# Kernel tuning notes

Measured on AMD Instinct MI355X. Metric: run time of the kernel, lower is better.

## Reference

```python
import jax, jax.numpy as jnp
import numpy as np

BPTT, BSZ, NTOKEN = 32, 32, 2000
NINP, NHID = 1024, 256


def setup_inputs() -> dict:
    key = jax.random.key(0)
    ks = jax.random.split(key, 8)
    s = 0.1  # matches uniform(-0.1, 0.1) init scale
    return {
        "input": jax.random.normal(ks[0], (BPTT, BSZ, NTOKEN), jnp.float32),
        "b": jax.random.normal(ks[1], (BSZ, NHID), jnp.float32),
        "RBF_w": jax.random.uniform(ks[2], (NINP, NTOKEN), jnp.float32, -s, s),
        "RBF_b": jnp.zeros((NINP,), jnp.float32),
        "emb_w": jax.random.uniform(ks[3], (NHID, NINP), jnp.float32, -s, s),
        "emb_b": jnp.zeros((NHID,), jnp.float32),
        "wfef_w": jax.random.uniform(ks[4], (NHID * NHID, NHID), jnp.float32, -s, s),
        "wfef_b": jnp.zeros((NHID * NHID,), jnp.float32),
        "dec_w": jax.random.uniform(ks[5], (NTOKEN, NHID), jnp.float32, -s, s),
        "dec_b": jnp.zeros((NTOKEN,), jnp.float32),
    }


def reference(input, b, RBF_w, RBF_b, emb_w, emb_b, wfef_w, wfef_b, dec_w, dec_b):
    bptt, bsz, ntoken = input.shape
    nhid = b.shape[1]
    ninp = RBF_w.shape[0]
    rbf_scale = np.float32(np.sqrt(2.0) / np.sqrt(ninp))
    # random Fourier features: cos(RBF(x)) * sqrt(2/ninp)
    encoded = jnp.cos(input @ RBF_w.T + RBF_b) * rbf_scale      # [bptt,bsz,ninp]
    obs = encoded @ emb_w.T + emb_b                              # [bptt,bsz,nhid]

    def step(b_t, obs_t):
        # per-sample transition matrix from current state
        W = (b_t @ wfef_w.T + wfef_b).reshape(bsz, nhid, nhid)   # [bsz,nhid,nhid]
        bn = jnp.einsum('brc,bc->br', W, obs_t)                  # [bsz,nhid]
        bn = bn / jnp.sqrt(jnp.sum(bn * bn, axis=1, keepdims=True))
        out = bn @ dec_w.T + dec_b                               # [bsz,ntoken]
        return bn, out

    b_final, outputs = jax.lax.scan(step, b, obs)                # outputs: [bptt,bsz,ntoken]
    return outputs, b_final
```

## Files before the change

kernel.cpp:

```cpp
#include <hip/hip_runtime.h>
#include <hip/hip_fp16.h>
#include <math.h>

typedef _Float16 half_t;
typedef __attribute__((ext_vector_type(2))) _Float16 f16x2;
typedef __attribute__((ext_vector_type(4))) _Float16 f16x4;
typedef __attribute__((ext_vector_type(8))) _Float16 f16x8;
typedef __attribute__((ext_vector_type(4))) float f32x4;

#define BPTT 32
#define BSZ 32
#define NTOK 2000
#define NTOKP 2048
#define NINP 1024
#define NHID 256
#define TB 1024
#define NH2 65536
#define TCH 8
#define FUSED_LDS 25600
#define FRONT_LDS 24576

__device__ __forceinline__ int swz(int row, int hoff) {
  return (row * 32 + hoff) ^ ((row & 7) << 3);
}

__global__ void cvtAll_k(const float* __restrict__ input, half_t* __restrict__ A1hi,
                         half_t* __restrict__ A1lo, const float* __restrict__ RBF_w,
                         half_t* __restrict__ B1hi, half_t* __restrict__ B1lo,
                         const float* __restrict__ emb_w,
                         const float* __restrict__ wfef_b,
                         const float* __restrict__ dec_w, half_t* __restrict__ B2,
                         half_t* __restrict__ WBh, half_t* __restrict__ B4) {
  int bid = blockIdx.x;
  if (bid < 16384) {
    const float* src;
    half_t *hi, *lo;
    int idx;
    if (bid < 8192) {
      src = input; hi = A1hi; lo = A1lo; idx = bid * 256 + threadIdx.x;
    } else {
      src = RBF_w; hi = B1hi; lo = B1lo; idx = (bid - 8192) * 256 + threadIdx.x;
    }
    int r = idx >> 11, c = idx & 2047;
    float v = (c < NTOK) ? src[(size_t)r * NTOK + c] : 0.f;
    half_t h = (half_t)v;
    hi[idx] = h;
    lo[idx] = (half_t)(v - (float)h);
    return;
  }
  int i = (bid - 16384) * 256 + threadIdx.x;
  if (i < 262144) { B2[i] = (half_t)emb_w[i]; return; }
  i -= 262144;
  if (i < 65536) { WBh[i] = (half_t)wfef_b[i]; return; }
  i -= 65536;
  int r = i >> 8, c = i & 255;
  B4[i] = (half_t)((r < NTOK) ? dec_w[(size_t)r * 256 + c] : 0.f);
}

template <int EP>
__global__ __launch_bounds__(256) void gemm128_k(const half_t* __restrict__ A,
                                                 const half_t* __restrict__ B,
                                                 void* __restrict__ C,
                                                 const float* __restrict__ bias, int K,
                                                 int ldc) {
  __shared__ half_t As[128 * 32];
  __shared__ half_t Bs[128 * 32];
  const int tid = threadIdx.x;
  const int lane = tid & 63, wave = tid >> 6;
  const int wr = wave >> 1, wc = wave & 1;
  const int row0 = blockIdx.x * 128, col0 = blockIdx.y * 128;
  const int srow = tid >> 2, sseg = tid & 3;
  const size_t aoff = (size_t)(row0 + srow) * K + sseg * 8;
  const size_t boff = (size_t)(col0 + srow) * K + sseg * 8;
  const int fr = lane & 15, fq = lane >> 4;

  f32x4 acc[4][4];
#pragma unroll
  for (int m = 0; m < 4; m++)
#pragma unroll
    for (int n = 0; n < 4; n++) acc[m][n] = (f32x4)(0.0f);

  for (int k0 = 0; k0 < K; k0 += 32) {
    f16x8 a0 = *(const f16x8*)(A + aoff + k0);
    f16x8 a1 = *(const f16x8*)(A + aoff + (size_t)64 * K + k0);
    f16x8 b0 = *(const f16x8*)(B + boff + k0);
    f16x8 b1 = *(const f16x8*)(B + boff + (size_t)64 * K + k0);
    __syncthreads();
    *(f16x8*)(As + swz(srow, sseg * 8)) = a0;
    *(f16x8*)(As + swz(srow + 64, sseg * 8)) = a1;
    *(f16x8*)(Bs + swz(srow, sseg * 8)) = b0;
    *(f16x8*)(Bs + swz(srow + 64, sseg * 8)) = b1;
    __syncthreads();
    f16x8 af[4], bf[4];
#pragma unroll
    for (int m = 0; m < 4; m++)
      af[m] = *(const f16x8*)(As + swz(wr * 64 + m * 16 + fr, fq * 8));
#pragma unroll
    for (int n = 0; n < 4; n++)
      bf[n] = *(const f16x8*)(Bs + swz(wc * 64 + n * 16 + fr, fq * 8));
#pragma unroll
    for (int m = 0; m < 4; m++)
#pragma unroll
      for (int n = 0; n < 4; n++)
        acc[m][n] = __builtin_amdgcn_mfma_f32_16x16x32_f16(af[m], bf[n], acc[m][n], 0, 0, 0);
  }

#pragma unroll
  for (int m = 0; m < 4; m++)
#pragma unroll
    for (int n = 0; n < 4; n++)
#pragma unroll
      for (int j = 0; j < 4; j++) {
        int gr = row0 + wr * 64 + m * 16 + fq * 4 + j;
        int gc = col0 + wc * 64 + n * 16 + fr;
        float v = acc[m][n][j];
        if (EP == 1) {
          ((half_t*)C)[(size_t)gr * ldc + gc] = (half_t)(v + bias[gc]);
        } else {
          ((float*)C)[(size_t)gr * ldc + gc] = v;
        }
      }
}

template <int EP>
__device__ __forceinline__ void gemmMC_body(const half_t* __restrict__ A,
                                            const half_t* __restrict__ B,
                                            void* __restrict__ C,
                                            const float* __restrict__ bias, int col0,
                                            int ldc, int nvalid, char* smem) {
  half_t* As = (half_t*)smem;
  half_t* Bs = (half_t*)(smem + 16384);
  const int tid = threadIdx.x;
  const int lane = tid & 63, wave = tid >> 6;
  const int wr = wave >> 2, wc = wave & 3;
  const int srow = tid >> 2, sseg = tid & 3;
  const int fr = lane & 15, fq = lane >> 4;
  const size_t aoff = (size_t)srow * 256 + sseg * 8;
  const size_t boff = (size_t)(col0 + (srow & 127)) * 256 + sseg * 8;

  f32x4 acc[4][2];
#pragma unroll
  for (int m = 0; m < 4; m++)
#pragma unroll
    for (int n = 0; n < 2; n++) acc[m][n] = (f32x4)(0.0f);

  for (int k0 = 0; k0 < 256; k0 += 32) {
    f16x8 a0 = *(const f16x8*)(A + aoff + k0);
    f16x8 b0;
    if (tid < 512) b0 = *(const f16x8*)(B + boff + k0);
    __syncthreads();
    *(f16x8*)(As + swz(srow, sseg * 8)) = a0;
    if (tid < 512) *(f16x8*)(Bs + swz(srow, sseg * 8)) = b0;
    __syncthreads();
    f16x8 af[4], bf[2];
#pragma unroll
    for (int m = 0; m < 4; m++)
      af[m] = *(const f16x8*)(As + swz(wr * 64 + m * 16 + fr, fq * 8));
#pragma unroll
    for (int n = 0; n < 2; n++)
      bf[n] = *(const f16x8*)(Bs + swz(wc * 32 + n * 16 + fr, fq * 8));
#pragma unroll
    for (int m = 0; m < 4; m++)
#pragma unroll
      for (int n = 0; n < 2; n++)
        acc[m][n] = __builtin_amdgcn_mfma_f32_16x16x32_f16(af[m], bf[n], acc[m][n], 0, 0, 0);
  }

#pragma unroll
  for (int m = 0; m < 4; m++)
#pragma unroll
    for (int n = 0; n < 2; n++)
#pragma unroll
      for (int j = 0; j < 4; j++) {
        int gr = wr * 64 + m * 16 + fq * 4 + j;
        int gc = col0 + wc * 32 + n * 16 + fr;
        if (EP == 0) {
          ((half_t*)C)[(size_t)gr * ldc + gc] = (half_t)acc[m][n][j];
        } else {
          if (gc < nvalid)
            ((float*)C)[(size_t)gr * ldc + gc] = acc[m][n][j] + bias[gc];
        }
      }
}

__device__ void scan_body(const half_t* __restrict__ Mc, const float* __restrict__ V,
                          int t0, const float* __restrict__ bin,
                          float* __restrict__ bstate, half_t* __restrict__ BN,
                          float* __restrict__ bfinal, int b, char* smem) {
  float(*Vs)[256] = (float(*)[256])smem;
  float(*partial)[260] = (float(*)[260])(smem + 8192);
  unsigned* bh2 = (unsigned*)(smem + 24832);
  float* red = (float*)(smem + 25344);
  const int tid = threadIdx.x;
  const int hh = tid >> 6, lane = tid & 63;
  const int hpar = lane >> 5, r8 = (lane & 31) * 8;

  if (tid < TCH * 64) {
    int vr = tid >> 6;
    *(f32x4*)&Vs[vr][lane * 4] =
        *(const f32x4*)(V + ((size_t)(t0 + vr) * 32 + b) * 256 + lane * 4);
  }
  if (tid < 128) {
    const float* bs = bin + b * 256 + tid * 2;
    union { f16x2 h; unsigned u; } z;
    z.h[0] = (half_t)bs[0];
    z.h[1] = (half_t)bs[1];
    bh2[tid] = z.u;
  }

  const half_t* mbase = Mc + (size_t)b * NH2 + (size_t)(hh * 16 + hpar) * 256 + r8;
  f16x8 cur[8], nxt[8];
#pragma unroll
  for (int k = 0; k < 8; k++) cur[k] = *(const f16x8*)(mbase + k * 512);
  __syncthreads();

  for (int tt = 0; tt < TCH; tt++) {
    const int tn = (tt < TCH - 1) ? tt + 1 : TCH - 1;
    const half_t* mb2 = mbase + (size_t)tn * 32 * NH2;
#pragma unroll
    for (int k = 0; k < 8; k++) nxt[k] = *(const f16x8*)(mb2 + k * 512);

    uint4 q0 = *(const uint4*)&bh2[hh * 8];
    uint4 q1 = *(const uint4*)&bh2[hh * 8 + 4];
    unsigned bu[8] = {q0.x, q0.y, q0.z, q0.w, q1.x, q1.y, q1.z, q1.w};
    const int sh = hpar * 16;
    half_t hv[8];
#pragma unroll
    for (int k = 0; k < 8; k++)
      hv[k] = __builtin_bit_cast(half_t, (unsigned short)(bu[k] >> sh));

    float a[8] = {0.f, 0.f, 0.f, 0.f, 0.f, 0.f, 0.f, 0.f};
#pragma unroll
    for (int k = 0; k < 8; k++)
#pragma unroll
      for (int j = 0; j < 8; j++) a[j] += (float)cur[k][j] * (float)hv[k];
#pragma unroll
    for (int j = 0; j < 8; j++) a[j] += __shfl_xor(a[j], 32);
    f32x4 st = hpar ? (f32x4){a[4], a[5], a[6], a[7]} : (f32x4){a[0], a[1], a[2], a[3]};
    *(f32x4*)&partial[hh][r8 + hpar * 4] = st;
    __syncthreads();

    float s = 0.f;
    if (tid < 256) {
#pragma unroll
      for (int g = 0; g < 16; g++) s += partial[g][tid];
      s += Vs[tt][tid];
      float sq = s * s;
#pragma unroll
      for (int o = 32; o > 0; o >>= 1) sq += __shfl_xor(sq, o);
      if ((tid & 63) == 0) red[tid >> 6] = sq;
    }
    __syncthreads();
    if (tid < 256) {
      float sumsq = red[0] + red[1] + red[2] + red[3];
      float bnv = s / sqrtf(sumsq);
      float bnv_hi = __shfl_down(bnv, 1);
      if (!(tid & 1)) {
        union { f16x2 h; unsigned u; } z;
        z.h[0] = (half_t)bnv;
        z.h[1] = (half_t)bnv_hi;
        bh2[tid >> 1] = z.u;
        *(unsigned*)(BN + ((size_t)(t0 + tt) * 32 + b) * 256 + tid) = z.u;
      }
      if (tt == TCH - 1) bstate[b * 256 + tid] = bnv;
      if (t0 + tt == BPTT - 1) bfinal[b * 256 + tid] = bnv;
    }
    __syncthreads();
#pragma unroll
    for (int k = 0; k < 8; k++) cur[k] = nxt[k];
  }
}

__global__ __launch_bounds__(1024) void fused_k(
    int scanN, int gemmN, const half_t* __restrict__ Msc,
    const float* __restrict__ Vbuf, int t0, const float* __restrict__ bin,
    float* __restrict__ bstate, half_t* __restrict__ BN,
    float* __restrict__ bfinal, const half_t* __restrict__ Ag,
    const half_t* __restrict__ Bg, half_t* __restrict__ Cg, int decRow0,
    const half_t* __restrict__ BNa, const half_t* __restrict__ B4,
    float* __restrict__ outp, const float* __restrict__ dec_b) {
  extern __shared__ char smem[];
  const int id = blockIdx.x;
  if (id < scanN) {
    scan_body(Msc, Vbuf, t0, bin, bstate, BN, bfinal, id, smem);
  } else if (id < scanN + gemmN) {
    const int g = id - scanN;
    gemmMC_body<0>(Ag, Bg, (void*)Cg, nullptr, g * 128, NH2, 0, smem);
  } else {
    const int d = id - scanN - gemmN;
    const int r0 = decRow0 + (d >> 4) * 256;
    gemmMC_body<3>(BNa + (size_t)r0 * 256, B4, (void*)(outp + (size_t)r0 * NTOK),
                   dec_b, (d & 15) * 128, NTOK, NTOK, smem);
  }
}

__global__ __launch_bounds__(256) void front_k(const half_t* __restrict__ Ahi,
                                               const half_t* __restrict__ Alo,
                                               const half_t* __restrict__ Bhi,
                                               const half_t* __restrict__ Blo,
                                               float* __restrict__ P,
                                               const float* __restrict__ wfef,
                                               half_t* __restrict__ wwt) {
  extern __shared__ char fsm[];
  if (blockIdx.x >= 512) {
    float(*tile)[33] = (float(*)[33])fsm;
    int id2 = blockIdx.x - 512;
    int r = id2 & 255, cb = (id2 >> 8) & 7, hb = id2 >> 11;
    int tx = threadIdx.x & 31, ty = threadIdx.x >> 5;
#pragma unroll
    for (int ii = 0; ii < 4; ii++) {
      int cl = ty + ii * 8;
      tile[cl][tx] = wfef[((size_t)(r * 256 + cb * 32 + cl)) * 256 + hb * 32 + tx];
    }
    __syncthreads();
#pragma unroll
    for (int ii = 0; ii < 4; ii++) {
      int hl = ty + ii * 8;
      wwt[((size_t)(hb * 32 + hl) * 256 + r) * 256 + cb * 32 + tx] =
          (half_t)tile[tx][hl];
    }
    return;
  }
  half_t* Ash = (half_t*)fsm;
  half_t* Asl = (half_t*)(fsm + 8192);
  half_t* Bsh = (half_t*)(fsm + 16384);
  half_t* Bsl = (half_t*)(fsm + 20480);
  const int id = blockIdx.x;
  const int kp = id & 3, r2 = id >> 2;
  const int bx = r2 & 7, by = r2 >> 3;
  const int row0 = bx * 128, col0 = by * 64, koff = kp * 512;
  const int tid = threadIdx.x;
  const int lane = tid & 63, wave = tid >> 6;
  const int wr = wave >> 1, wc = wave & 1;
  const int srow = tid >> 2, sseg = tid & 3;
  const size_t aoff = (size_t)(row0 + srow) * NTOKP + koff + sseg * 8;
  const size_t boff = (size_t)(col0 + srow) * NTOKP + koff + sseg * 8;
  const int fr = lane & 15, fq = lane >> 4;

  f32x4 acc[4][2];
#pragma unroll
  for (int m = 0; m < 4; m++)
#pragma unroll
    for (int n = 0; n < 2; n++) acc[m][n] = (f32x4)(0.0f);

  for (int k0 = 0; k0 < 512; k0 += 32) {
    f16x8 ah0 = *(const f16x8*)(Ahi + aoff + k0);
    f16x8 ah1 = *(const f16x8*)(Ahi + aoff + (size_t)64 * NTOKP + k0);
    f16x8 al0 = *(const f16x8*)(Alo + aoff + k0);
    f16x8 al1 = *(const f16x8*)(Alo + aoff + (size_t)64 * NTOKP + k0);
    f16x8 bh0 = *(const f16x8*)(Bhi + boff + k0);
    f16x8 bl0 = *(const f16x8*)(Blo + boff + k0);
    __syncthreads();
    *(f16x8*)(Ash + swz(srow, sseg * 8)) = ah0;
    *(f16x8*)(Ash + swz(srow + 64, sseg * 8)) = ah1;
    *(f16x8*)(Asl + swz(srow, sseg * 8)) = al0;
    *(f16x8*)(Asl + swz(srow + 64, sseg * 8)) = al1;
    *(f16x8*)(Bsh + swz(srow, sseg * 8)) = bh0;
    *(f16x8*)(Bsl + swz(srow, sseg * 8)) = bl0;
    __syncthreads();
    f16x8 afh[4], afl[4], bfh[2], bfl[2];
#pragma unroll
    for (int m = 0; m < 4; m++) {
      afh[m] = *(const f16x8*)(Ash + swz(wr * 64 + m * 16 + fr, fq * 8));
      afl[m] = *(const f16x8*)(Asl + swz(wr * 64 + m * 16 + fr, fq * 8));
    }
#pragma unroll
    for (int n = 0; n < 2; n++) {
      bfh[n] = *(const f16x8*)(Bsh + swz(wc * 32 + n * 16 + fr, fq * 8));
      bfl[n] = *(const f16x8*)(Bsl + swz(wc * 32 + n * 16 + fr, fq * 8));
    }
#pragma unroll
    for (int m = 0; m < 4; m++)
#pragma unroll
      for (int n = 0; n < 2; n++) {
        acc[m][n] = __builtin_amdgcn_mfma_f32_16x16x32_f16(afh[m], bfh[n], acc[m][n], 0, 0, 0);
        acc[m][n] = __builtin_amdgcn_mfma_f32_16x16x32_f16(afl[m], bfh[n], acc[m][n], 0, 0, 0);
        acc[m][n] = __builtin_amdgcn_mfma_f32_16x16x32_f16(afh[m], bfl[n], acc[m][n], 0, 0, 0);
      }
  }

  float* Pk = P + (size_t)kp * (NINP * (size_t)TB);
#pragma unroll
  for (int m = 0; m < 4; m++)
#pragma unroll
    for (int n = 0; n < 2; n++)
#pragma unroll
      for (int j = 0; j < 4; j++) {
        int gr = row0 + wr * 64 + m * 16 + fq * 4 + j;
        int gc = col0 + wc * 32 + n * 16 + fr;
        Pk[(size_t)gr * NINP + gc] = acc[m][n][j];
      }
}

__global__ void rbf_combine_k(const float* __restrict__ P, const float* __restrict__ bias,
                              half_t* __restrict__ C) {
  int idx = blockIdx.x * 256 + threadIdx.x;
  int e0 = idx * 4;
  int col = e0 & (NINP - 1);
  f32x4 s = *(const f32x4*)(P + e0);
  s += *(const f32x4*)(P + (size_t)1 * TB * NINP + e0);
  s += *(const f32x4*)(P + (size_t)2 * TB * NINP + e0);
  s += *(const f32x4*)(P + (size_t)3 * TB * NINP + e0);
  const float RBF_SCALE = 0.04419417382415922f;
  f16x4 o;
#pragma unroll
  for (int j = 0; j < 4; j++) o[j] = (half_t)(cosf(s[j] + bias[col + j]) * RBF_SCALE);
  *(f16x4*)(C + e0) = o;
}


extern "C" void kernel_launch(void* const* d_in, const int* in_sizes, int n_in,
                              void* d_out, int out_size, void* d_ws, size_t ws_size,
                              hipStream_t stream) {
  const float* input = (const float*)d_in[0];
  const float* b0 = (const float*)d_in[1];
  const float* RBF_w = (const float*)d_in[2];
  const float* RBF_b = (const float*)d_in[3];
  const float* emb_w = (const float*)d_in[4];
  const float* emb_b = (const float*)d_in[5];
  const float* wfef_w = (const float*)d_in[6];
  const float* wfef_b = (const float*)d_in[7];
  const float* dec_w = (const float*)d_in[8];
  const float* dec_b = (const float*)d_in[9];

  char* ws = (char*)d_ws;
  size_t off = 0;
  auto alloc = [&](size_t bytes) {
    void* p = ws + off;
    off += (bytes + 255) & ~(size_t)255;
    return p;
  };
  half_t* A1hi = (half_t*)alloc((size_t)TB * NTOKP * 2);
  half_t* A1lo = (half_t*)alloc((size_t)TB * NTOKP * 2);
  half_t* B1hi = (half_t*)alloc((size_t)NINP * NTOKP * 2);
  half_t* B1lo = (half_t*)alloc((size_t)NINP * NTOKP * 2);
  half_t* encA = (half_t*)alloc((size_t)TB * NINP * 2);
  half_t* B2 = (half_t*)alloc((size_t)NHID * NINP * 2);
  half_t* obsA = (half_t*)alloc((size_t)TB * NHID * 2);
  half_t* WBh = (half_t*)alloc((size_t)NHID * NHID * 2);
  half_t* B4 = (half_t*)alloc((size_t)2048 * NHID * 2);
  float* Vbuf = (float*)alloc((size_t)TB * NHID * 4);
  half_t* BN = (half_t*)alloc((size_t)TB * NHID * 2);
  float* bstate = (float*)alloc((size_t)BSZ * NHID * 4);
  half_t* WWT = (half_t*)alloc((size_t)NH2 * NHID * 2);
  half_t* Mmat = (half_t*)alloc((size_t)TB * NH2 * 2);
  if (off > ws_size) return;

  float* Pk = (float*)Mmat;

  float* outp = (float*)d_out;
  float* bfinal = outp + (size_t)TB * NTOK;

  cvtAll_k<<<19712, 256, 0, stream>>>(input, A1hi, A1lo, RBF_w, B1hi, B1lo, emb_w,
                                      wfef_b, dec_w, B2, WBh, B4);
  front_k<<<512 + 16384, 256, FRONT_LDS, stream>>>(A1hi, A1lo, B1hi, B1lo, Pk,
                                                   wfef_w, WWT);
  rbf_combine_k<<<(TB * NINP / 4) / 256, 256, 0, stream>>>(Pk, RBF_b, encA);
  gemm128_k<1><<<dim3(8, 2), 256, 0, stream>>>(encA, B2, obsA, emb_b, NINP, NHID);
  gemm128_k<2><<<dim3(8, 2), 256, 0, stream>>>(obsA, WBh, Vbuf, nullptr, NHID, NHID);

  fused_k<<<512, 1024, FUSED_LDS, stream>>>(
      0, 512, nullptr, Vbuf, 0, b0, bstate, BN, bfinal, obsA, WWT, Mmat, 0, BN, B4,
      outp, dec_b);
  for (int tc = 0; tc < 3; tc++) {
    fused_k<<<544, 1024, FUSED_LDS, stream>>>(
        32, 512, Mmat + (size_t)tc * 256 * NH2, Vbuf, tc * TCH,
        (tc == 0) ? b0 : bstate, bstate, BN, bfinal,
        obsA + (size_t)(tc + 1) * 256 * NHID, WWT, Mmat + (size_t)(tc + 1) * 256 * NH2,
        0, BN, B4, outp, dec_b);
  }
  fused_k<<<32 + 48, 1024, FUSED_LDS, stream>>>(
      32, 0, Mmat + (size_t)3 * 256 * NH2, Vbuf, 3 * TCH, bstate, bstate, BN, bfinal,
      nullptr, nullptr, nullptr, 0, BN, B4, outp, dec_b);
  fused_k<<<16, 1024, FUSED_LDS, stream>>>(
      0, 0, nullptr, Vbuf, 0, bstate, bstate, BN, bfinal, nullptr, nullptr, nullptr,
      768, BN, B4, outp, dec_b);
}
```

Baseline: 229.2 us.

## Vectorize wfef transpose tiles and overlap decoder GEMM chunks with later scan launches

The wfef transpose blocks now handle 64x64 tiles with float4 loads, an XOR-swizzled LDS layout and 8-wide half stores, which cuts the block count from 16384 to 4096 and widens memory transactions. The launch schedule is also restructured: decoder output blocks for earlier timestep chunks are folded into the later fused scan/GEMM launches (extra 16 blocks with decRow0 offsets), so the decoder no longer sits in a serialized tail. The trade-off is larger per-launch grids that may compete for CUs with the latency-critical scan blocks.

```diff
diff --git a/kernel.cpp b/kernel.cpp
--- a/kernel.cpp
+++ b/kernel.cpp
@@ -303,21 +303,29 @@
                                                half_t* __restrict__ wwt) {
   extern __shared__ char fsm[];
   if (blockIdx.x >= 512) {
-    float(*tile)[33] = (float(*)[33])fsm;
-    int id2 = blockIdx.x - 512;
-    int r = id2 & 255, cb = (id2 >> 8) & 7, hb = id2 >> 11;
-    int tx = threadIdx.x & 31, ty = threadIdx.x >> 5;
-#pragma unroll
-    for (int ii = 0; ii < 4; ii++) {
-      int cl = ty + ii * 8;
-      tile[cl][tx] = wfef[((size_t)(r * 256 + cb * 32 + cl)) * 256 + hb * 32 + tx];
-    }
-    __syncthreads();
-#pragma unroll
-    for (int ii = 0; ii < 4; ii++) {
-      int hl = ty + ii * 8;
-      wwt[((size_t)(hb * 32 + hl) * 256 + r) * 256 + cb * 32 + tx] =
-          (half_t)tile[tx][hl];
+    float* tile = (float*)fsm;
+    const int p = blockIdx.x - 512;
+    const int r = p & 255, cb = (p >> 8) & 3, hb = p >> 10;
+    const int tid = threadIdx.x;
+    const int l16 = tid & 15, cr = tid >> 4;
+#pragma unroll
+    for (int i = 0; i < 4; i++) {
+      int c = i * 16 + cr;
+      int m = ((c >> 3) & 7) << 3;
+      f32x4 v = *(const f32x4*)(wfef + ((size_t)(r * 256 + cb * 64 + c)) * 256 +
+                                hb * 64 + l16 * 4);
+      *(f32x4*)&tile[c * 64 + ((l16 * 4) ^ m)] = v;
+    }
+    __syncthreads();
+    const int cg = tid & 7, hr = tid >> 3;
+#pragma unroll
+    for (int i = 0; i < 2; i++) {
+      int h = i * 32 + hr;
+      int hs = h ^ (cg << 3);
+      f16x8 o;
+#pragma unroll
+      for (int j = 0; j < 8; j++) o[j] = (half_t)tile[(cg * 8 + j) * 64 + hs];
+      *(f16x8*)(wwt + ((size_t)(hb * 64 + h) * 256 + r) * 256 + cb * 64 + cg * 8) = o;
     }
     return;
   }
@@ -453,8 +461,8 @@
 
   cvtAll_k<<<19712, 256, 0, stream>>>(input, A1hi, A1lo, RBF_w, B1hi, B1lo, emb_w,
                                       wfef_b, dec_w, B2, WBh, B4);
-  front_k<<<512 + 16384, 256, FRONT_LDS, stream>>>(A1hi, A1lo, B1hi, B1lo, Pk,
-                                                   wfef_w, WWT);
+  front_k<<<512 + 4096, 256, FRONT_LDS, stream>>>(A1hi, A1lo, B1hi, B1lo, Pk,
+                                                  wfef_w, WWT);
   rbf_combine_k<<<(TB * NINP / 4) / 256, 256, 0, stream>>>(Pk, RBF_b, encA);
   gemm128_k<1><<<dim3(8, 2), 256, 0, stream>>>(encA, B2, obsA, emb_b, NINP, NHID);
   gemm128_k<2><<<dim3(8, 2), 256, 0, stream>>>(obsA, WBh, Vbuf, nullptr, NHID, NHID);
@@ -462,16 +470,20 @@
   fused_k<<<512, 1024, FUSED_LDS, stream>>>(
       0, 512, nullptr, Vbuf, 0, b0, bstate, BN, bfinal, obsA, WWT, Mmat, 0, BN, B4,
       outp, dec_b);
-  for (int tc = 0; tc < 3; tc++) {
-    fused_k<<<544, 1024, FUSED_LDS, stream>>>(
-        32, 512, Mmat + (size_t)tc * 256 * NH2, Vbuf, tc * TCH,
-        (tc == 0) ? b0 : bstate, bstate, BN, bfinal,
-        obsA + (size_t)(tc + 1) * 256 * NHID, WWT, Mmat + (size_t)(tc + 1) * 256 * NH2,
-        0, BN, B4, outp, dec_b);
-  }
-  fused_k<<<32 + 48, 1024, FUSED_LDS, stream>>>(
-      32, 0, Mmat + (size_t)3 * 256 * NH2, Vbuf, 3 * TCH, bstate, bstate, BN, bfinal,
-      nullptr, nullptr, nullptr, 0, BN, B4, outp, dec_b);
+  fused_k<<<544, 1024, FUSED_LDS, stream>>>(
+      32, 512, Mmat, Vbuf, 0, b0, bstate, BN, bfinal, obsA + (size_t)256 * NHID, WWT,
+      Mmat + (size_t)256 * NH2, 0, BN, B4, outp, dec_b);
+  fused_k<<<560, 1024, FUSED_LDS, stream>>>(
+      32, 512, Mmat + (size_t)256 * NH2, Vbuf, TCH, bstate, bstate, BN, bfinal,
+      obsA + (size_t)512 * NHID, WWT, Mmat + (size_t)512 * NH2, 0, BN, B4, outp,
+      dec_b);
+  fused_k<<<560, 1024, FUSED_LDS, stream>>>(
+      32, 512, Mmat + (size_t)512 * NH2, Vbuf, 2 * TCH, bstate, bstate, BN, bfinal,
+      obsA + (size_t)768 * NHID, WWT, Mmat + (size_t)768 * NH2, 256, BN, B4, outp,
+      dec_b);
+  fused_k<<<48, 1024, FUSED_LDS, stream>>>(
+      32, 0, Mmat + (size_t)768 * NH2, Vbuf, 3 * TCH, bstate, bstate, BN, bfinal,
+      nullptr, nullptr, nullptr, 512, BN, B4, outp, dec_b);
   fused_k<<<16, 1024, FUSED_LDS, stream>>>(
       0, 0, nullptr, Vbuf, 0, bstate, bstate, BN, bfinal, nullptr, nullptr, nullptr,
       768, BN, B4, outp, dec_b);
```

After: 224.3 us. 2.1% less time.
